# Kernel tuning notes

Hardware: AMD Instinct MI355X
Metric: run time of the kernel (lower is better)

## Reference

```python
import jax, jax.numpy as jnp
import numpy as np

EMBED_DIM = 1024
HEAD_DIM = 64


def setup_inputs() -> dict:
    key = jax.random.key(0)
    k1, k2, k3, k4 = jax.random.split(key, 4)
    B, T = 4, 4096
    x = jax.random.normal(k1, (B, T, EMBED_DIM), dtype=jnp.float32)
    # nn.Linear(EMBED_DIM, head_dim, bias=False): store as (EMBED_DIM, head_dim)
    s = (1.0 / np.sqrt(EMBED_DIM)).astype(np.float32)
    Wk = jax.random.uniform(k2, (EMBED_DIM, HEAD_DIM), jnp.float32, -s, s)
    Wq = jax.random.uniform(k3, (EMBED_DIM, HEAD_DIM), jnp.float32, -s, s)
    Wv = jax.random.uniform(k4, (EMBED_DIM, HEAD_DIM), jnp.float32, -s, s)
    return {"x": x, "Wq": Wq, "Wk": Wk, "Wv": Wv}


def reference(x, Wq, Wk, Wv):
    B, T, E = x.shape
    q = jnp.einsum('bte,ed->btd', x, Wq)  # (B,T,D)
    k = jnp.einsum('bte,ed->btd', x, Wk)
    v = jnp.einsum('bte,ed->btd', x, Wv)
    # NOTE: original scales by EMBED_DIM**-0.5 (x.size(-1)), not head_dim**-0.5
    scale = jnp.asarray(E, x.dtype) ** -0.5
    scores = jnp.einsum('bqd,bkd->bqk', q, k) * scale  # (B,T,T)
    causal = jnp.tril(jnp.ones((T, T), dtype=bool))
    scores = jnp.where(causal, scores, jnp.asarray(-jnp.inf, scores.dtype))
    attn = jax.nn.softmax(scores, axis=-1)
    # dropout is identity at inference (deterministic baseline)
    out = jnp.einsum('bqk,bkd->bqd', attn, v)  # (B,T,D)
    return out
```

## Files before the change

### kernel.cpp

```cpp
#include <hip/hip_runtime.h>
#include <hip/hip_bf16.h>
#include <stdint.h>

#define BATCH 4
#define SEQ   4096
#define EMB   1024
#define HD    64

typedef __bf16 bf16x8 __attribute__((ext_vector_type(8)));
typedef float  f32x4  __attribute__((ext_vector_type(4)));
typedef unsigned short u16;

union ABFrag { u16 s[8]; bf16x8 v; };

__device__ __forceinline__ u16 f2bf_rne(float f) {
    union { float f; uint32_t u; } cv; cv.f = f;
    uint32_t u = cv.u;
    return (u16)((u + 0x7fffu + ((u >> 16) & 1u)) >> 16);
}
__device__ __forceinline__ float bf2f(u16 h) {
    union { uint32_t u; float f; } cv; cv.u = ((uint32_t)h) << 16;
    return cv.f;
}
__device__ __forceinline__ void gld16(const void* g, void* l) {
    __builtin_amdgcn_global_load_lds(
        (const __attribute__((address_space(1))) void*)g,
        (__attribute__((address_space(3))) void*)l, 16, 0, 0);
}

__global__ __launch_bounds__(256) void wt_kernel(
        const float* __restrict__ Wq, const float* __restrict__ Wk,
        const float* __restrict__ Wv, u16* __restrict__ Wt) {
    int idx = blockIdx.x * 256 + threadIdx.x;
    int i = idx >> 16;
    int r = idx & 65535;
    int n = r >> 10;
    int k = r & 1023;
    const float* W = (i == 0) ? Wq : (i == 1) ? Wk : Wv;
    Wt[idx] = f2bf_rne(W[k * HD + n]);
}

__global__ __launch_bounds__(256) void qkv_kernel(
        const float* __restrict__ x, const u16* __restrict__ Wt,
        u16* __restrict__ Qw, u16* __restrict__ Kw, u16* __restrict__ Vt) {
    __shared__ float xs[2][2048];
    __shared__ u16   wsb[2][12288];

    const int t    = threadIdx.x;
    const int wave = t >> 6;
    const int lane = t & 63;
    const int m16  = lane & 15;
    const int quad = lane >> 4;
    const int rh   = wave & 1;
    const int ch   = wave >> 1;
    const int R0   = blockIdx.x * 32;

    #define ISSUE(buf_, kt_) do {                                              \
        const int r4_ = lane >> 4, c16_ = lane & 15;                           \
        _Pragma("unroll")                                                      \
        for (int j_ = 0; j_ < 2; ++j_) {                                       \
            const int ii_  = wave + (j_ << 2);                                 \
            const int row_ = (ii_ << 2) + r4_;                      \
            const int kc_  = c16_ ^ (row_ & 15);                               \
            gld16(x + (size_t)(R0 + row_) * EMB + ((kt_) << 6) + (kc_ << 2),   \
                  &xs[buf_][ii_ << 8]);                                        \
        }                                                                      \
        const int r8_ = lane >> 3, c8_ = lane & 7;                             \
        _Pragma("unroll")                                                      \
        for (int j_ = 0; j_ < 6; ++j_) {                                       \
            const int rb_ = (wave * 6 + j_) << 3;                  \
            const int kw_ = c8_ ^ r8_;                                         \
            gld16(Wt + (size_t)(rb_ + r8_) * 1024 + ((kt_) << 6) + (kw_ << 3), \
                  &wsb[buf_][(wave * 6 + j_) << 9]);                           \
        }                                                                      \
    } while (0)

    f32x4 acc[6];
#pragma unroll
    for (int a = 0; a < 6; ++a) acc[a] = (f32x4){0.f, 0.f, 0.f, 0.f};

    const int row_x = rh * 16 + m16;
    ISSUE(0, 0);

    for (int kt = 0; kt < 16; ++kt) {
        const int buf = kt & 1;
        __syncthreads();
        if (kt < 15) ISSUE(buf ^ 1, kt + 1);

#pragma unroll
        for (int ks2 = 0; ks2 < 2; ++ks2) {
            const int c0 = (ks2 << 3) + (quad << 1);
            const float4 a0 = *(const float4*)&xs[buf][(row_x << 6) + ((c0 ^ m16) << 2)];
            const float4 a1 = *(const float4*)&xs[buf][(row_x << 6) + (((c0 + 1) ^ m16) << 2)];
            ABFrag af;
            af.s[0] = f2bf_rne(a0.x); af.s[1] = f2bf_rne(a0.y);
            af.s[2] = f2bf_rne(a0.z); af.s[3] = f2bf_rne(a0.w);
            af.s[4] = f2bf_rne(a1.x); af.s[5] = f2bf_rne(a1.y);
            af.s[6] = f2bf_rne(a1.z); af.s[7] = f2bf_rne(a1.w);
#pragma unroll
            for (int i = 0; i < 6; ++i) {
                const int tt   = ch * 6 + i;
                const int rowW = (tt << 4) + m16;
                const bf16x8 bf = *(const bf16x8*)&wsb[buf][
                        (rowW << 6) + ((((ks2 << 2) + quad) ^ (m16 & 7)) << 3)];
                acc[i] = __builtin_amdgcn_mfma_f32_16x16x32_bf16(af.v, bf, acc[i], 0, 0, 0);
            }
        }
    }
    #undef ISSUE

    const int rowbase = R0 + rh * 16 + (quad << 2);
    const int bidx = rowbase >> 12;
    const int t0   = rowbase & 4095;
#pragma unroll
    for (int i = 0; i < 6; ++i) {
        const int tt  = ch * 6 + i;
        const int w3  = tt >> 2;
        const int col = ((tt & 3) << 4) + m16;
        if (w3 == 0) {
#pragma unroll
            for (int reg = 0; reg < 4; ++reg)
                Qw[(size_t)(rowbase + reg) * HD + col] = f2bf_rne(acc[i][reg] * 0.03125f);
        } else if (w3 == 1) {
#pragma unroll
            for (int reg = 0; reg < 4; ++reg)
                Kw[(size_t)(rowbase + reg) * HD + col] = f2bf_rne(acc[i][reg]);
        } else {
            ushort4 vv;
            vv.x = f2bf_rne(acc[i][0]); vv.y = f2bf_rne(acc[i][1]);
            vv.z = f2bf_rne(acc[i][2]); vv.w = f2bf_rne(acc[i][3]);
            *(ushort4*)(Vt + (size_t)((bidx << 6) + col) * SEQ + t0) = vv;
        }
    }
}

__global__ __launch_bounds__(256) void attn_part_kernel(
        const u16* __restrict__ Qw, const u16* __restrict__ Kw,
        const u16* __restrict__ Vt, u16* __restrict__ Opart,
        float* __restrict__ Mp, float* __restrict__ Lp) {
    __shared__ u16 kv[2][2][4096];
    __shared__ u16 ldsP[4][16 * 72];

    const int pid = blockIdx.x;
    const int r   = pid >> 8;
    const int i   = pid & 255;
    const int b   = i & 3;
    const int h   = i >> 2;
    const int qt  = h ^ (int)((0x1f203f00u >> (r * 8)) & 63u);
    const int c   = r;
    const int p_out = (((b << 6) + qt) << 2) + c;

    const int wave = threadIdx.x >> 6;
    const int lane = threadIdx.x & 63;
    const int m16  = lane & 15;
    const int quad = lane >> 4;

    #define ISSUE_KV(buf_, jt_) do {                                           \
        const int r8_ = lane >> 3, c8_ = lane & 7;                             \
        const int kc_ = c8_ ^ r8_;                                             \
        _Pragma("unroll")                                                      \
        for (int j_ = 0; j_ < 2; ++j_) {                                       \
            const int row_ = ((wave * 2 + j_) << 3) + r8_;          \
            gld16(Kw + ((size_t)(b * SEQ + ((jt_) << 6) + row_) << 6) + (kc_ << 3), \
                  &kv[buf_][0][(wave * 2 + j_) << 9]);                         \
            gld16(Vt + (size_t)((b << 6) + row_) * SEQ + ((jt_) << 6) + (kc_ << 3), \
                  &kv[buf_][1][(wave * 2 + j_) << 9]);                         \
        }                                                                      \
    } while (0)

    const int qrow = (qt << 6) + (wave << 4) + m16;
    const u16* qbase = Qw + ((size_t)(b * SEQ + qrow) << 6);
    const bf16x8 qf0 = *(const bf16x8*)(qbase + (quad << 3));
    const bf16x8 qf1 = *(const bf16x8*)(qbase + 32 + (quad << 3));

    f32x4 acc[4];
#pragma unroll
    for (int dt = 0; dt < 4; ++dt) acc[dt] = (f32x4){0.f, 0.f, 0.f, 0.f};
    float m_i = -3.0e38f;
    float l_i = 0.f;

    u16* ldsW = &ldsP[wave][0];
    const int xs0 = (quad ^ (m16 & 7)) << 3;
    const int xs1 = (((quad + 4)) ^ (m16 & 7)) << 3;

    if (c <= qt) ISSUE_KV(0, c);

    int buf = 0;
    for (int jt = c; jt <= qt; jt += 4) {
        __syncthreads();
        if (jt + 4 <= qt) ISSUE_KV(buf ^ 1, jt + 4);

        f32x4 s[4];
#pragma unroll
        for (int mt = 0; mt < 4; ++mt) {
            const int base = ((mt << 4) + m16) << 6;
            bf16x8 k0 = *(const bf16x8*)&kv[buf][0][base + xs0];
            bf16x8 k1 = *(const bf16x8*)&kv[buf][0][base + xs1];
            s[mt] = (f32x4){0.f, 0.f, 0.f, 0.f};
            s[mt] = __builtin_amdgcn_mfma_f32_16x16x32_bf16(k0, qf0, s[mt], 0, 0, 0);
            s[mt] = __builtin_amdgcn_mfma_f32_16x16x32_bf16(k1, qf1, s[mt], 0, 0, 0);
        }

        if (jt == qt) {
            const int q_in = (wave << 4) + m16;
#pragma unroll
            for (int mt = 0; mt < 4; ++mt) {
                const int k_in = (mt << 4) + (quad << 2);
#pragma unroll
                for (int reg = 0; reg < 4; ++reg)
                    if (k_in + reg > q_in) s[mt][reg] = -3.0e38f;
            }
        }

        float tm = fmaxf(fmaxf(s[0][0], s[0][1]), fmaxf(s[0][2], s[0][3]));
#pragma unroll
        for (int mt = 1; mt < 4; ++mt)
            tm = fmaxf(tm, fmaxf(fmaxf(s[mt][0], s[mt][1]), fmaxf(s[mt][2], s[mt][3])));
        tm = fmaxf(tm, __shfl_xor(tm, 16));
        tm = fmaxf(tm, __shfl_xor(tm, 32));

        const float mnew  = fmaxf(m_i, tm);
        const float alpha = __expf(m_i - mnew);
        m_i = mnew;

        float psum = 0.f;
#pragma unroll
        for (int mt = 0; mt < 4; ++mt) {
            const float p0 = __expf(s[mt][0] - mnew);
            const float p1 = __expf(s[mt][1] - mnew);
            const float p2 = __expf(s[mt][2] - mnew);
            const float p3 = __expf(s[mt][3] - mnew);
            psum += (p0 + p1) + (p2 + p3);
            ushort4 pv;
            pv.x = f2bf_rne(p0); pv.y = f2bf_rne(p1);
            pv.z = f2bf_rne(p2); pv.w = f2bf_rne(p3);
            *(ushort4*)(ldsW + m16 * 72 + (mt << 4) + (quad << 2)) = pv;
        }
        l_i = l_i * alpha + psum;
#pragma unroll
        for (int dt = 0; dt < 4; ++dt)
#pragma unroll
            for (int reg = 0; reg < 4; ++reg) acc[dt][reg] *= alpha;

        const bf16x8 p0 = *(const bf16x8*)(ldsW + m16 * 72 + (quad << 3));
        const bf16x8 p1 = *(const bf16x8*)(ldsW + m16 * 72 + 32 + (quad << 3));
#pragma unroll
        for (int dt = 0; dt < 4; ++dt) {
            const int base = ((dt << 4) + m16) << 6;
            bf16x8 v0 = *(const bf16x8*)&kv[buf][1][base + xs0];
            bf16x8 v1 = *(const bf16x8*)&kv[buf][1][base + xs1];
            acc[dt] = __builtin_amdgcn_mfma_f32_16x16x32_bf16(v0, p0, acc[dt], 0, 0, 0);
            acc[dt] = __builtin_amdgcn_mfma_f32_16x16x32_bf16(v1, p1, acc[dt], 0, 0, 0);
        }
        buf ^= 1;
    }
    #undef ISSUE_KV

    float l = l_i;
    l += __shfl_xor(l, 16);
    l += __shfl_xor(l, 32);

    u16* ob = Opart + (size_t)p_out * 4096;
    const int qin = (wave << 4) + m16;
#pragma unroll
    for (int dt = 0; dt < 4; ++dt) {
        ushort4 vv;
        vv.x = f2bf_rne(acc[dt][0]); vv.y = f2bf_rne(acc[dt][1]);
        vv.z = f2bf_rne(acc[dt][2]); vv.w = f2bf_rne(acc[dt][3]);
        *(ushort4*)(ob + qin * 64 + (dt << 4) + (quad << 2)) = vv;
    }
    if (quad == 0) {
        Mp[p_out * 64 + qin] = m_i;
        Lp[p_out * 64 + qin] = l;
    }
}

__global__ __launch_bounds__(256) void combine_kernel(
        const u16* __restrict__ Opart, const float* __restrict__ Mp,
        const float* __restrict__ Lp, float* __restrict__ out) {
    __shared__ float sm[4][16];
    __shared__ float sl[4][16];
    const int bq = blockIdx.x >> 2;
    const int rq = blockIdx.x & 3;
    const int pidbase = bq << 2;
    const int t = threadIdx.x;
    if (t < 64) {
        const int cc = t >> 4, rr = t & 15;
        sm[cc][rr] = Mp[(pidbase + cc) * 64 + rq * 16 + rr];
        sl[cc][rr] = Lp[(pidbase + cc) * 64 + rq * 16 + rr];
    }
    __syncthreads();

    const int row_l = t >> 4;
    const int c4    = (t & 15) << 2;
    const int row   = rq * 16 + row_l;

    const float M = fmaxf(fmaxf(sm[0][row_l], sm[1][row_l]),
                          fmaxf(sm[2][row_l], sm[3][row_l]));
    float n0 = 0.f, n1 = 0.f, n2 = 0.f, n3 = 0.f, den = 0.f;
#pragma unroll
    for (int cc = 0; cc < 4; ++cc) {
        const float w = __expf(sm[cc][row_l] - M);
        den += w * sl[cc][row_l];
        const ushort4 op = *(const ushort4*)&Opart[
                (size_t)(pidbase + cc) * 4096 + row * 64 + c4];
        n0 += w * bf2f(op.x); n1 += w * bf2f(op.y);
        n2 += w * bf2f(op.z); n3 += w * bf2f(op.w);
    }
    const float rd = 1.0f / den;
    float4 o; o.x = n0 * rd; o.y = n1 * rd; o.z = n2 * rd; o.w = n3 * rd;
    *(float4*)&out[((size_t)bq << 12) + (row << 6) + c4] = o;
}

extern "C" void kernel_launch(void* const* d_in, const int* in_sizes, int n_in,
                              void* d_out, int out_size, void* d_ws, size_t ws_size,
                              hipStream_t stream) {
    const float* x  = (const float*)d_in[0];
    const float* Wq = (const float*)d_in[1];
    const float* Wk = (const float*)d_in[2];
    const float* Wv = (const float*)d_in[3];
    float* out = (float*)d_out;

    char* ws = (char*)d_ws;
    u16* Qw    = (u16*)(ws);
    u16* Kw    = (u16*)(ws + (2u << 20));
    u16* Vt    = (u16*)(ws + (4u << 20));
    u16* Wt    = (u16*)(ws + (6u << 20));
    u16* Opart = (u16*)(ws + (13u << 19));
    float* Mp  = (float*)(ws + (29u << 19));
    float* Lp  = (float*)(ws + (59u << 18));

    wt_kernel<<<768, 256, 0, stream>>>(Wq, Wk, Wv, Wt);
    qkv_kernel<<<512, 256, 0, stream>>>(x, Wt, Qw, Kw, Vt);
    attn_part_kernel<<<1024, 256, 0, stream>>>(Qw, Kw, Vt, Opart, Mp, Lp);
    combine_kernel<<<1024, 256, 0, stream>>>(Opart, Mp, Lp, out);
}
```

Before: 150.8 us.

## Restructure QKV projection to keep one full weight matrix resident in LDS

The QKV projection kernel now assigns each block one of the three weight matrices, loads it fully into LDS once, and streams x rows directly from global memory into registers without double-buffered LDS staging. Each wave computes two 16-row tiles against all 64 output columns. This removes per-k-step barriers and repeated weight staging, but x is now read three times (once per weight) and only 192 blocks are launched.

```diff
diff --git a/kernel.cpp b/kernel.cpp
--- a/kernel.cpp
+++ b/kernel.cpp
@@ -40,96 +40,92 @@
     Wt[idx] = f2bf_rne(W[k * HD + n]);
 }
 
-__global__ __launch_bounds__(256) void qkv_kernel(
+__global__ __launch_bounds__(512) void qkv_kernel(
         const float* __restrict__ x, const u16* __restrict__ Wt,
         u16* __restrict__ Qw, u16* __restrict__ Kw, u16* __restrict__ Vt) {
-    __shared__ float xs[2][2048];
-    __shared__ u16   wsb[2][12288];
+    __shared__ u16 wl[64 * 1032];
 
     const int t    = threadIdx.x;
     const int wave = t >> 6;
     const int lane = t & 63;
     const int m16  = lane & 15;
     const int quad = lane >> 4;
-    const int rh   = wave & 1;
-    const int ch   = wave >> 1;
-    const int R0   = blockIdx.x * 32;
-
-    #define ISSUE(buf_, kt_) do {                                              \
-        const int r4_ = lane >> 4, c16_ = lane & 15;                           \
-        _Pragma("unroll")                                                      \
-        for (int j_ = 0; j_ < 2; ++j_) {                                       \
-            const int ii_  = wave + (j_ << 2);                                 \
-            const int row_ = (ii_ << 2) + r4_;                      \
-            const int kc_  = c16_ ^ (row_ & 15);                               \
-            gld16(x + (size_t)(R0 + row_) * EMB + ((kt_) << 6) + (kc_ << 2),   \
-                  &xs[buf_][ii_ << 8]);                                        \
-        }                                                                      \
-        const int r8_ = lane >> 3, c8_ = lane & 7;                             \
-        _Pragma("unroll")                                                      \
-        for (int j_ = 0; j_ < 6; ++j_) {                                       \
-            const int rb_ = (wave * 6 + j_) << 3;                  \
-            const int kw_ = c8_ ^ r8_;                                         \
-            gld16(Wt + (size_t)(rb_ + r8_) * 1024 + ((kt_) << 6) + (kw_ << 3), \
-                  &wsb[buf_][(wave * 6 + j_) << 9]);                           \
-        }                                                                      \
-    } while (0)
-
-    f32x4 acc[6];
-#pragma unroll
-    for (int a = 0; a < 6; ++a) acc[a] = (f32x4){0.f, 0.f, 0.f, 0.f};
-
-    const int row_x = rh * 16 + m16;
-    ISSUE(0, 0);
-
-    for (int kt = 0; kt < 16; ++kt) {
-        const int buf = kt & 1;
-        __syncthreads();
-        if (kt < 15) ISSUE(buf ^ 1, kt + 1);
-
-#pragma unroll
-        for (int ks2 = 0; ks2 < 2; ++ks2) {
-            const int c0 = (ks2 << 3) + (quad << 1);
-            const float4 a0 = *(const float4*)&xs[buf][(row_x << 6) + ((c0 ^ m16) << 2)];
-            const float4 a1 = *(const float4*)&xs[buf][(row_x << 6) + (((c0 + 1) ^ m16) << 2)];
-            ABFrag af;
-            af.s[0] = f2bf_rne(a0.x); af.s[1] = f2bf_rne(a0.y);
-            af.s[2] = f2bf_rne(a0.z); af.s[3] = f2bf_rne(a0.w);
-            af.s[4] = f2bf_rne(a1.x); af.s[5] = f2bf_rne(a1.y);
-            af.s[6] = f2bf_rne(a1.z); af.s[7] = f2bf_rne(a1.w);
-#pragma unroll
-            for (int i = 0; i < 6; ++i) {
-                const int tt   = ch * 6 + i;
-                const int rowW = (tt << 4) + m16;
-                const bf16x8 bf = *(const bf16x8*)&wsb[buf][
-                        (rowW << 6) + ((((ks2 << 2) + quad) ^ (m16 & 7)) << 3)];
-                acc[i] = __builtin_amdgcn_mfma_f32_16x16x32_bf16(af.v, bf, acc[i], 0, 0, 0);
+    const int wv   = blockIdx.x >> 6;
+    const int rb   = blockIdx.x & 63;
+
+    {
+        const u16* wsrc = Wt + (wv << 16);
+#pragma unroll
+        for (int j = 0; j < 16; ++j) {
+            const int idx = (wave << 4) + j;
+            const int n   = idx >> 1;
+            const int hh  = idx & 1;
+            gld16(wsrc + (n << 10) + (hh << 9) + (lane << 3),
+                  &wl[n * 1032 + (hh << 9)]);
+        }
+    }
+    __syncthreads();
+
+    const int rtA  = (rb << 4) + (wave << 1);
+    const int rowA = (rtA << 4) + m16;
+    const float* xpA = x + (size_t)rowA * EMB + (quad << 3);
+    const float* xpB = xpA + (16 * EMB);
+
+    f32x4 accA[4], accB[4];
+#pragma unroll
+    for (int tt = 0; tt < 4; ++tt) {
+        accA[tt] = (f32x4){0.f, 0.f, 0.f, 0.f};
+        accB[tt] = (f32x4){0.f, 0.f, 0.f, 0.f};
+    }
+
+    const u16* wbase = &wl[m16 * 1032 + (quad << 3)];
+
+#pragma unroll 2
+    for (int kt = 0; kt < 32; ++kt) {
+        const float4 a0A = *(const float4*)(xpA + (kt << 5));
+        const float4 a1A = *(const float4*)(xpA + (kt << 5) + 4);
+        const float4 a0B = *(const float4*)(xpB + (kt << 5));
+        const float4 a1B = *(const float4*)(xpB + (kt << 5) + 4);
+        ABFrag afA, afB;
+        afA.s[0] = f2bf_rne(a0A.x); afA.s[1] = f2bf_rne(a0A.y);
+        afA.s[2] = f2bf_rne(a0A.z); afA.s[3] = f2bf_rne(a0A.w);
+        afA.s[4] = f2bf_rne(a1A.x); afA.s[5] = f2bf_rne(a1A.y);
+        afA.s[6] = f2bf_rne(a1A.z); afA.s[7] = f2bf_rne(a1A.w);
+        afB.s[0] = f2bf_rne(a0B.x); afB.s[1] = f2bf_rne(a0B.y);
+        afB.s[2] = f2bf_rne(a0B.z); afB.s[3] = f2bf_rne(a0B.w);
+        afB.s[4] = f2bf_rne(a1B.x); afB.s[5] = f2bf_rne(a1B.y);
+        afB.s[6] = f2bf_rne(a1B.z); afB.s[7] = f2bf_rne(a1B.w);
+#pragma unroll
+        for (int tt = 0; tt < 4; ++tt) {
+            const bf16x8 bf = *(const bf16x8*)(wbase + tt * (16 * 1032) + (kt << 5));
+            accA[tt] = __builtin_amdgcn_mfma_f32_16x16x32_bf16(afA.v, bf, accA[tt], 0, 0, 0);
+            accB[tt] = __builtin_amdgcn_mfma_f32_16x16x32_bf16(afB.v, bf, accB[tt], 0, 0, 0);
+        }
+    }
+
+#pragma unroll
+    for (int half = 0; half < 2; ++half) {
+        const f32x4* acc = half ? accB : accA;
+        const int rowbase = ((rtA + half) << 4) + (quad << 2);
+        const int bidx = rowbase >> 12;
+        const int t0   = rowbase & 4095;
+#pragma unroll
+        for (int tt = 0; tt < 4; ++tt) {
+            const int col = (tt << 4) + m16;
+            if (wv == 0) {
+#pragma unroll
+                for (int reg = 0; reg < 4; ++reg)
+                    Qw[(size_t)(rowbase + reg) * HD + col] = f2bf_rne(acc[tt][reg] * 0.03125f);
+            } else if (wv == 1) {
+#pragma unroll
+                for (int reg = 0; reg < 4; ++reg)
+                    Kw[(size_t)(rowbase + reg) * HD + col] = f2bf_rne(acc[tt][reg]);
+            } else {
+                ushort4 vv;
+                vv.x = f2bf_rne(acc[tt][0]); vv.y = f2bf_rne(acc[tt][1]);
+                vv.z = f2bf_rne(acc[tt][2]); vv.w = f2bf_rne(acc[tt][3]);
+                *(ushort4*)(Vt + (size_t)((bidx << 6) + col) * SEQ + t0) = vv;
             }
-        }
-    }
-    #undef ISSUE
-
-    const int rowbase = R0 + rh * 16 + (quad << 2);
-    const int bidx = rowbase >> 12;
-    const int t0   = rowbase & 4095;
-#pragma unroll
-    for (int i = 0; i < 6; ++i) {
-        const int tt  = ch * 6 + i;
-        const int w3  = tt >> 2;
-        const int col = ((tt & 3) << 4) + m16;
-        if (w3 == 0) {
-#pragma unroll
-            for (int reg = 0; reg < 4; ++reg)
-                Qw[(size_t)(rowbase + reg) * HD + col] = f2bf_rne(acc[i][reg] * 0.03125f);
-        } else if (w3 == 1) {
-#pragma unroll
-            for (int reg = 0; reg < 4; ++reg)
-                Kw[(size_t)(rowbase + reg) * HD + col] = f2bf_rne(acc[i][reg]);
-        } else {
-            ushort4 vv;
-            vv.x = f2bf_rne(acc[i][0]); vv.y = f2bf_rne(acc[i][1]);
-            vv.z = f2bf_rne(acc[i][2]); vv.w = f2bf_rne(acc[i][3]);
-            *(ushort4*)(Vt + (size_t)((bidx << 6) + col) * SEQ + t0) = vv;
         }
     }
 }
@@ -331,7 +327,7 @@
     float* Lp  = (float*)(ws + (59u << 18));
 
     wt_kernel<<<768, 256, 0, stream>>>(Wq, Wk, Wv, Wt);
-    qkv_kernel<<<512, 256, 0, stream>>>(x, Wt, Qw, Kw, Vt);
+    qkv_kernel<<<192, 512, 0, stream>>>(x, Wt, Qw, Kw, Vt);
     attn_part_kernel<<<1024, 256, 0, stream>>>(Qw, Kw, Vt, Opart, Mp, Lp);
     combine_kernel<<<1024, 256, 0, stream>>>(Opart, Mp, Lp, out);
 }
```

New measurement: 160.1 us. 6.2% more time.
